# Optimization experiments

Hardware: AMD Instinct MI355X
Metric: run time of the kernel (lower is better)

Reference implementation:

```python
import jax, jax.numpy as jnp
import numpy as np

# Static configuration (mirrors init_kwargs)
F_REAL = 64
F_CAT = 32
OUT = 32
HID = [64, 64, 32]
IDX_REAL_MISS = np.arange(16)   # indices into the real-feature subset
IDX_CAT_MISS = np.arange(8)     # indices into the cat-feature subset
N_CAT_MISS = len(IDX_CAT_MISS)
B = 8192


def wn(v, g):
    """PyTorch weight_norm: w = g * v / ||v|| with norm over input dim (last axis).
    v: [F, out, in], g: [F, out] -> w: [F, out, in]"""
    return g[..., None] * v / jnp.linalg.norm(v, axis=-1, keepdims=True)


def setup_inputs() -> dict:
    key = jax.random.key(0)
    ks = jax.random.split(key, 16)
    s = 0.3
    values = jax.random.normal(ks[0], (B, 96), dtype=jnp.float32)
    miss = (jax.random.uniform(ks[1], (B, 96)) < 0.1).astype(jnp.float32)
    tabular = jnp.stack([values, miss], axis=1)  # [B, 2, 96]
    # Per-feature weight-normed MLP params, stacked over F_REAL features.
    inp = {
        "tabular": tabular,
        "v0": jax.random.normal(ks[2], (F_REAL, HID[0], 1)) * s,
        "g0": jnp.ones((F_REAL, HID[0])),
        "b0": jax.random.normal(ks[3], (F_REAL, HID[0])) * 0.01,
        "v1": jax.random.normal(ks[4], (F_REAL, HID[1], HID[0])) * s,
        "g1": jnp.ones((F_REAL, HID[1])),
        "b1": jax.random.normal(ks[5], (F_REAL, HID[1])) * 0.01,
        "v2": jax.random.normal(ks[6], (F_REAL, HID[2], HID[1])) * s,
        "g2": jnp.ones((F_REAL, HID[2])),
        "b2": jax.random.normal(ks[7], (F_REAL, HID[2])) * 0.01,
        "v3": jax.random.normal(ks[8], (F_REAL, OUT, HID[2])) * s,
        "g3": jnp.ones((F_REAL, OUT)),
        "cat_linear": jax.random.normal(ks[9], (F_CAT, OUT)) * s,
        "missing_emb": jax.random.normal(ks[10], (len(IDX_REAL_MISS) + N_CAT_MISS, OUT)) * s,
        "bias": jnp.zeros((1, OUT)),
    }
    return inp


def reference(tabular, v0, g0, b0, v1, g1, b1, v2, g2, b2, v3, g3,
              cat_linear, missing_emb, bias):
    # Eval mode: nn.Dropout / nn.Dropout1d are identity.
    values, is_missing = tabular[:, 0], tabular[:, 1]
    val_real, miss_real = values[:, :F_REAL], is_missing[:, :F_REAL]
    val_cat, miss_cat = values[:, F_REAL:F_REAL + F_CAT], is_missing[:, F_REAL:F_REAL + F_CAT]

    # Batched tiny MLPs over all real features at once.
    w0 = wn(v0, g0)[:, :, 0]                  # [F, H0] (scalar input)
    h = jax.nn.relu(val_real[:, :, None] * w0[None] + b0[None])        # [B,F,H0]
    h = jax.nn.relu(jnp.einsum('bfi,foi->bfo', h, wn(v1, g1)) + b1[None])  # [B,F,H1]
    h = jax.nn.relu(jnp.einsum('bfi,foi->bfo', h, wn(v2, g2)) + b2[None])  # [B,F,H2]
    feat_real = jnp.einsum('bfi,foi->bfo', h, wn(v3, g3))               # [B,F,OUT]

    feat_cat = cat_linear[None] * val_cat[:, :, None]                   # [B,Fc,OUT]

    feat_real = feat_real * (1.0 - miss_real[:, :, None])
    feat_cat = feat_cat * (1.0 - miss_cat[:, :, None])

    # Scatter-fill missing embeddings (add is exact since masked entries are zero)
    feat_real = feat_real.at[:, IDX_REAL_MISS, :].add(
        missing_emb[N_CAT_MISS:][None] * miss_real[:, IDX_REAL_MISS, None])
    feat_cat = feat_cat.at[:, IDX_CAT_MISS, :].add(
        missing_emb[:N_CAT_MISS][None] * miss_cat[:, IDX_CAT_MISS, None])

    features = jnp.concatenate([feat_real, feat_cat], axis=1)           # [B,96,OUT]
    logits = jnp.sum(features, axis=1) + bias                           # [B,OUT]
    return (logits, features)
```

## Files before the change

kernel.cpp:

```cpp
#include <hip/hip_runtime.h>
#include <math.h>

typedef _Float16 f16;
typedef _Float16 f16x8 __attribute__((ext_vector_type(8)));
typedef float f32x4 __attribute__((ext_vector_type(4)));

#define NB 8192
#define LOGN (NB * 32)

#define OFF_B1 16384
#define OFF_B2 540672
#define OFF_B3 802816
#define OFF_PART 933888

__global__ void prep_weights(const float* __restrict__ v0, const float* __restrict__ g0,
                             const float* __restrict__ v1, const float* __restrict__ g1,
                             const float* __restrict__ v2, const float* __restrict__ g2,
                             const float* __restrict__ v3, const float* __restrict__ g3,
                             float* __restrict__ w0, f16* __restrict__ b1f,
                             f16* __restrict__ b2f, f16* __restrict__ b3f) {
    int t = blockIdx.x * blockDim.x + threadIdx.x;
    if (t < 4096) {
        float v = v0[t];
        w0[t] = g0[t] * (v >= 0.f ? 1.f : -1.f);
    } else if (t < 8192) {
        int r = t - 4096;
        int f = r >> 6, n = r & 63;
        const float* vp = v1 + (size_t)r * 64;
        float ss = 0.f;
        #pragma unroll
        for (int i = 0; i < 64; ++i) ss += vp[i] * vp[i];
        float scale = g1[r] * __frsqrt_rn(ss);
        f16* dst = b1f + f * 4096;
        #pragma unroll
        for (int k = 0; k < 64; ++k) {
            int lane = (n & 15) | (((k & 31) >> 3) << 4);
            dst[(k >> 5) * 2048 + (n >> 4) * 512 + lane * 8 + (k & 7)] = (f16)(vp[k] * scale);
        }
    } else if (t < 10240) {
        int r = t - 8192;
        int f = r >> 5, n = r & 31;
        const float* vp = v2 + (size_t)r * 64;
        float ss = 0.f;
        #pragma unroll
        for (int i = 0; i < 64; ++i) ss += vp[i] * vp[i];
        float scale = g2[r] * __frsqrt_rn(ss);
        f16* dst = b2f + f * 2048;
        #pragma unroll
        for (int k = 0; k < 64; ++k) {
            int lane = (n & 15) | (((k & 31) >> 3) << 4);
            dst[(k >> 5) * 1024 + (n >> 4) * 512 + lane * 8 + (k & 7)] = (f16)(vp[k] * scale);
        }
    } else if (t < 12288) {
        int r = t - 10240;
        int f = r >> 5, n = r & 31;
        const float* vp = v3 + (size_t)r * 32;
        float ss = 0.f;
        #pragma unroll
        for (int i = 0; i < 32; ++i) ss += vp[i] * vp[i];
        float scale = g3[r] * __frsqrt_rn(ss);
        f16* dst = b3f + f * 1024;
        #pragma unroll
        for (int k = 0; k < 32; ++k) {
            int lane = (n & 15) | ((k >> 3) << 4);
            dst[(n >> 4) * 512 + lane * 8 + (k & 7)] = (f16)(vp[k] * scale);
        }
    }
}

__global__ __launch_bounds__(256, 2)
void nam_real_mfma(const float* __restrict__ tab, const float* __restrict__ w0,
                   const f16* __restrict__ b1f, const f16* __restrict__ b2f,
                   const f16* __restrict__ b3f,
                   const float* __restrict__ b0, const float* __restrict__ b1,
                   const float* __restrict__ b2, const float* __restrict__ memb,
                   float* __restrict__ feat, float* __restrict__ part) {
    __shared__ char lds[4][8192];
    const int wave = threadIdx.x >> 6, lane = threadIdx.x & 63;
    const int lq = lane >> 4, lr = lane & 15;
    const int rowbase = blockIdx.x * 128 + wave * 32;
    const int f0 = blockIdx.y * 8;
    char* h1b = lds[wave];
    char* h2b = lds[wave] + 4096;

    float lacc[2][2][4];
    #pragma unroll
    for (int mt = 0; mt < 2; ++mt)
        #pragma unroll
        for (int nt = 0; nt < 2; ++nt)
            #pragma unroll
            for (int j = 0; j < 4; ++j) lacc[mt][nt][j] = 0.f;

    #pragma unroll 1
    for (int fi = 0; fi < 8; ++fi) {
        const int f = f0 + fi;

        f16x8 B1[2][4], B2[2][2], B3[2];
        {
            const f16* p1 = b1f + f * 4096 + lane * 8;
            #pragma unroll
            for (int ks = 0; ks < 2; ++ks)
                #pragma unroll
                for (int nt = 0; nt < 4; ++nt)
                    B1[ks][nt] = *(const f16x8*)(p1 + ks * 2048 + nt * 512);
            const f16* p2 = b2f + f * 2048 + lane * 8;
            #pragma unroll
            for (int ks = 0; ks < 2; ++ks)
                #pragma unroll
                for (int nt = 0; nt < 2; ++nt)
                    B2[ks][nt] = *(const f16x8*)(p2 + ks * 1024 + nt * 512);
            const f16* p3 = b3f + f * 1024 + lane * 8;
            #pragma unroll
            for (int nt = 0; nt < 2; ++nt)
                B3[nt] = *(const f16x8*)(p3 + nt * 512);
        }

        float b1v[4], b2v[2];
        #pragma unroll
        for (int nt = 0; nt < 4; ++nt) b1v[nt] = b1[f * 64 + nt * 16 + lr];
        #pragma unroll
        for (int nt = 0; nt < 2; ++nt) b2v[nt] = b2[f * 32 + nt * 16 + lr];
        float vmt[2];
        #pragma unroll
        for (int mt = 0; mt < 2; ++mt)
            vmt[mt] = tab[(size_t)(rowbase + mt * 16 + lr) * 192 + f];
        float ms[2][4];
        #pragma unroll
        for (int mt = 0; mt < 2; ++mt)
            #pragma unroll
            for (int j = 0; j < 4; ++j)
                ms[mt][j] = tab[(size_t)(rowbase + mt * 16 + lq * 4 + j) * 192 + 96 + f];

        f16x8 A0[2][2];
        #pragma unroll
        for (int ks = 0; ks < 2; ++ks) {
            float w0v[8], b0v[8];
            *(float4*)&w0v[0] = *(const float4*)(w0 + f * 64 + ks * 32 + lq * 8);
            *(float4*)&w0v[4] = *(const float4*)(w0 + f * 64 + ks * 32 + lq * 8 + 4);
            *(float4*)&b0v[0] = *(const float4*)(b0 + f * 64 + ks * 32 + lq * 8);
            *(float4*)&b0v[4] = *(const float4*)(b0 + f * 64 + ks * 32 + lq * 8 + 4);
            #pragma unroll
            for (int mt = 0; mt < 2; ++mt)
                #pragma unroll
                for (int i = 0; i < 8; ++i)
                    A0[mt][ks][i] = (f16)fmaxf(fmaf(vmt[mt], w0v[i], b0v[i]), 0.f);
        }

        f32x4 acc1[2][4];
        #pragma unroll
        for (int mt = 0; mt < 2; ++mt)
            #pragma unroll
            for (int nt = 0; nt < 4; ++nt) acc1[mt][nt] = (f32x4){0.f, 0.f, 0.f, 0.f};
        #pragma unroll
        for (int ks = 0; ks < 2; ++ks)
            #pragma unroll
            for (int nt = 0; nt < 4; ++nt)
                #pragma unroll
                for (int mt = 0; mt < 2; ++mt)
                    acc1[mt][nt] = __builtin_amdgcn_mfma_f32_16x16x32_f16(A0[mt][ks], B1[ks][nt], acc1[mt][nt], 0, 0, 0);
        #pragma unroll
        for (int mt = 0; mt < 2; ++mt)
            #pragma unroll
            for (int nt = 0; nt < 4; ++nt) {
                int n = nt * 16 + lr;
                int colb = ((n >> 3) << 4) + ((n & 7) << 1);
                #pragma unroll
                for (int j = 0; j < 4; ++j) {
                    int row = mt * 16 + lq * 4 + j;
                    int byte = ((row << 7) + colb) ^ ((row & 7) << 4);
                    *(f16*)(h1b + byte) = (f16)fmaxf(acc1[mt][nt][j] + b1v[nt], 0.f);
                }
            }

        f16x8 A1[2][2];
        #pragma unroll
        for (int mt = 0; mt < 2; ++mt)
            #pragma unroll
            for (int ks = 0; ks < 2; ++ks) {
                int row = mt * 16 + lr;
                int byte = ((row << 7) + ((ks * 4 + lq) << 4)) ^ ((row & 7) << 4);
                A1[mt][ks] = *(const f16x8*)(h1b + byte);
            }
        f32x4 acc2[2][2];
        #pragma unroll
        for (int mt = 0; mt < 2; ++mt)
            #pragma unroll
            for (int nt = 0; nt < 2; ++nt) acc2[mt][nt] = (f32x4){0.f, 0.f, 0.f, 0.f};
        #pragma unroll
        for (int ks = 0; ks < 2; ++ks)
            #pragma unroll
            for (int nt = 0; nt < 2; ++nt)
                #pragma unroll
                for (int mt = 0; mt < 2; ++mt)
                    acc2[mt][nt] = __builtin_amdgcn_mfma_f32_16x16x32_f16(A1[mt][ks], B2[ks][nt], acc2[mt][nt], 0, 0, 0);
        #pragma unroll
        for (int mt = 0; mt < 2; ++mt)
            #pragma unroll
            for (int nt = 0; nt < 2; ++nt) {
                int n = nt * 16 + lr;
                int colb = ((n >> 3) << 4) + ((n & 7) << 1);
                #pragma unroll
                for (int j = 0; j < 4; ++j) {
                    int row = mt * 16 + lq * 4 + j;
                    int byte = ((row << 7) + colb) ^ ((row & 7) << 4);
                    *(f16*)(h2b + byte) = (f16)fmaxf(acc2[mt][nt][j] + b2v[nt], 0.f);
                }
            }

        f16x8 A2[2];
        #pragma unroll
        for (int mt = 0; mt < 2; ++mt) {
            int row = mt * 16 + lr;
            int byte = ((row << 7) + (lq << 4)) ^ ((row & 7) << 4);
            A2[mt] = *(const f16x8*)(h2b + byte);
        }
        f32x4 acc3[2][2];
        #pragma unroll
        for (int mt = 0; mt < 2; ++mt)
            #pragma unroll
            for (int nt = 0; nt < 2; ++nt) acc3[mt][nt] = (f32x4){0.f, 0.f, 0.f, 0.f};
        #pragma unroll
        for (int nt = 0; nt < 2; ++nt)
            #pragma unroll
            for (int mt = 0; mt < 2; ++mt)
                acc3[mt][nt] = __builtin_amdgcn_mfma_f32_16x16x32_f16(A2[mt], B3[nt], acc3[mt][nt], 0, 0, 0);

        float e[2] = {0.f, 0.f};
        const bool hasemb = (f < 16);
        if (hasemb) {
            #pragma unroll
            for (int nt = 0; nt < 2; ++nt) e[nt] = memb[(8 + f) * 32 + nt * 16 + lr];
        }
        #pragma unroll
        for (int mt = 0; mt < 2; ++mt)
            #pragma unroll
            for (int nt = 0; nt < 2; ++nt) {
                int o = nt * 16 + lr;
                #pragma unroll
                for (int j = 0; j < 4; ++j) {
                    int row = rowbase + mt * 16 + lq * 4 + j;
                    float keep = 1.f - ms[mt][j];
                    float v = acc3[mt][nt][j] * keep;
                    if (hasemb) v = fmaf(e[nt], ms[mt][j], v);
                    feat[(size_t)row * 3072 + f * 32 + o] = v;
                    lacc[mt][nt][j] += v;
                }
            }
    }

    if (part) {
        float* pp = part + (size_t)blockIdx.y * LOGN;
        #pragma unroll
        for (int mt = 0; mt < 2; ++mt)
            #pragma unroll
            for (int nt = 0; nt < 2; ++nt)
                #pragma unroll
                for (int j = 0; j < 4; ++j) {
                    int row = rowbase + mt * 16 + lq * 4 + j;
                    pp[row * 32 + nt * 16 + lr] = lacc[mt][nt][j];
                }
    }
}

__global__ __launch_bounds__(256)
void nam_cat(const float* __restrict__ tab, const float* __restrict__ cat_linear,
             const float* __restrict__ memb, float* __restrict__ feat,
             float* __restrict__ part) {
    int t = blockIdx.x * blockDim.x + threadIdx.x;
    int o = t & 31;
    int b = t >> 5;
    const float* tb = tab + (size_t)b * 192;
    float sum = 0.f;
    #pragma unroll
    for (int fc = 0; fc < 32; ++fc) {
        float val = tb[64 + fc];
        float miss = tb[160 + fc];
        float r = cat_linear[fc * 32 + o] * val * (1.f - miss);
        if (fc < 8) r = fmaf(memb[fc * 32 + o], miss, r);
        feat[(size_t)b * 3072 + (64 + fc) * 32 + o] = r;
        sum += r;
    }
    if (part) part[8 * LOGN + t] = sum;
}

__global__ __launch_bounds__(256)
void nam_reduce(const float* __restrict__ part, const float* __restrict__ bias,
                float* __restrict__ logits) {
    int t = blockIdx.x * blockDim.x + threadIdx.x;
    float s = bias[t & 31];
    #pragma unroll
    for (int g = 0; g < 9; ++g) s += part[g * LOGN + t];
    logits[t] = s;
}

__global__ __launch_bounds__(256)
void nam_logits(const float* __restrict__ feat, const float* __restrict__ bias,
                float* __restrict__ logits) {
    int t = blockIdx.x * blockDim.x + threadIdx.x;
    int o = t & 31;
    int b = t >> 5;
    float s = bias[o];
    const float* fp = feat + (size_t)b * 3072 + o;
    #pragma unroll 8
    for (int f = 0; f < 96; ++f) s += fp[f * 32];
    logits[t] = s;
}

extern "C" void kernel_launch(void* const* d_in, const int* in_sizes, int n_in,
                              void* d_out, int out_size, void* d_ws, size_t ws_size,
                              hipStream_t stream) {
    const float* tab        = (const float*)d_in[0];
    const float* v0         = (const float*)d_in[1];
    const float* g0         = (const float*)d_in[2];
    const float* b0         = (const float*)d_in[3];
    const float* v1         = (const float*)d_in[4];
    const float* g1         = (const float*)d_in[5];
    const float* b1         = (const float*)d_in[6];
    const float* v2         = (const float*)d_in[7];
    const float* g2         = (const float*)d_in[8];
    const float* b2         = (const float*)d_in[9];
    const float* v3         = (const float*)d_in[10];
    const float* g3         = (const float*)d_in[11];
    const float* cat_linear = (const float*)d_in[12];
    const float* memb       = (const float*)d_in[13];
    const float* bias       = (const float*)d_in[14];

    float* out    = (float*)d_out;
    float* logits = out;
    float* feat   = out + LOGN;

    float* w0  = (float*)d_ws;
    f16*   b1f = (f16*)((char*)d_ws + OFF_B1);
    f16*   b2f = (f16*)((char*)d_ws + OFF_B2);
    f16*   b3f = (f16*)((char*)d_ws + OFF_B3);
    float* part = (float*)((char*)d_ws + OFF_PART);
    const bool use_part = ws_size >= (size_t)OFF_PART + 9ull * LOGN * 4ull;
    float* partp = use_part ? part : nullptr;

    prep_weights<<<48, 256, 0, stream>>>(v0, g0, v1, g1, v2, g2, v3, g3, w0, b1f, b2f, b3f);

    dim3 gr(64, 8);
    nam_real_mfma<<<gr, 256, 0, stream>>>(tab, w0, b1f, b2f, b3f, b0, b1, b2, memb, feat, partp);

    nam_cat<<<LOGN / 256, 256, 0, stream>>>(tab, cat_linear, memb, feat, partp);

    if (use_part)
        nam_reduce<<<LOGN / 256, 256, 0, stream>>>(part, bias, logits);
    else
        nam_logits<<<LOGN / 256, 256, 0, stream>>>(feat, bias, logits);
}
```

Baseline: 53.05 us.

## Split weight prep into parallel passes, stage tab in LDS, fuse cat with reduce

Weight prep is split in two. One kernel computes the per-row norm scales with float4 loads. A second kernel runs one thread per fp16 fragment element, replacing the serial per-row scatter writes. The MFMA kernel now stages its block's value and missing columns in shared memory once, instead of issuing strided global loads on every feature iteration. The categorical kernel also folds in the partial-sum reduction and bias, which removes one launch and one write and re-read of a partial buffer. The cost is an extra prep launch and a __syncthreads.

```diff
diff --git a/kernel.cpp b/kernel.cpp
--- a/kernel.cpp
+++ b/kernel.cpp
@@ -8,63 +8,84 @@
 #define NB 8192
 #define LOGN (NB * 32)
 
-#define OFF_B1 16384
-#define OFF_B2 540672
-#define OFF_B3 802816
-#define OFF_PART 933888
-
-__global__ void prep_weights(const float* __restrict__ v0, const float* __restrict__ g0,
-                             const float* __restrict__ v1, const float* __restrict__ g1,
-                             const float* __restrict__ v2, const float* __restrict__ g2,
-                             const float* __restrict__ v3, const float* __restrict__ g3,
-                             float* __restrict__ w0, f16* __restrict__ b1f,
-                             f16* __restrict__ b2f, f16* __restrict__ b3f) {
+#define OFF_W0   0
+#define OFF_SC1  16384
+#define OFF_SC2  32768
+#define OFF_SC3  40960
+#define OFF_B1   49152
+#define OFF_B2   573440
+#define OFF_B3   835584
+#define OFF_PART 966656
+#define WS_NEED  (OFF_PART + 8ull * LOGN * 4ull)
+
+__global__ __launch_bounds__(256)
+void prep_norm(const float* __restrict__ v0, const float* __restrict__ g0,
+               const float* __restrict__ v1, const float* __restrict__ g1,
+               const float* __restrict__ v2, const float* __restrict__ g2,
+               const float* __restrict__ v3, const float* __restrict__ g3,
+               float* __restrict__ ws) {
     int t = blockIdx.x * blockDim.x + threadIdx.x;
     if (t < 4096) {
         float v = v0[t];
-        w0[t] = g0[t] * (v >= 0.f ? 1.f : -1.f);
+        ws[OFF_W0 / 4 + t] = g0[t] * (v >= 0.f ? 1.f : -1.f);
     } else if (t < 8192) {
         int r = t - 4096;
-        int f = r >> 6, n = r & 63;
         const float* vp = v1 + (size_t)r * 64;
         float ss = 0.f;
         #pragma unroll
-        for (int i = 0; i < 64; ++i) ss += vp[i] * vp[i];
-        float scale = g1[r] * __frsqrt_rn(ss);
-        f16* dst = b1f + f * 4096;
-        #pragma unroll
-        for (int k = 0; k < 64; ++k) {
-            int lane = (n & 15) | (((k & 31) >> 3) << 4);
-            dst[(k >> 5) * 2048 + (n >> 4) * 512 + lane * 8 + (k & 7)] = (f16)(vp[k] * scale);
-        }
+        for (int i = 0; i < 16; ++i) {
+            float4 x = *(const float4*)(vp + i * 4);
+            ss += x.x * x.x + x.y * x.y + x.z * x.z + x.w * x.w;
+        }
+        ws[OFF_SC1 / 4 + r] = g1[r] * __frsqrt_rn(ss);
     } else if (t < 10240) {
         int r = t - 8192;
-        int f = r >> 5, n = r & 31;
         const float* vp = v2 + (size_t)r * 64;
         float ss = 0.f;
         #pragma unroll
-        for (int i = 0; i < 64; ++i) ss += vp[i] * vp[i];
-        float scale = g2[r] * __frsqrt_rn(ss);
-        f16* dst = b2f + f * 2048;
-        #pragma unroll
-        for (int k = 0; k < 64; ++k) {
-            int lane = (n & 15) | (((k & 31) >> 3) << 4);
-            dst[(k >> 5) * 1024 + (n >> 4) * 512 + lane * 8 + (k & 7)] = (f16)(vp[k] * scale);
-        }
+        for (int i = 0; i < 16; ++i) {
+            float4 x = *(const float4*)(vp + i * 4);
+            ss += x.x * x.x + x.y * x.y + x.z * x.z + x.w * x.w;
+        }
+        ws[OFF_SC2 / 4 + r] = g2[r] * __frsqrt_rn(ss);
     } else if (t < 12288) {
         int r = t - 10240;
-        int f = r >> 5, n = r & 31;
         const float* vp = v3 + (size_t)r * 32;
         float ss = 0.f;
         #pragma unroll
-        for (int i = 0; i < 32; ++i) ss += vp[i] * vp[i];
-        float scale = g3[r] * __frsqrt_rn(ss);
-        f16* dst = b3f + f * 1024;
-        #pragma unroll
-        for (int k = 0; k < 32; ++k) {
-            int lane = (n & 15) | ((k >> 3) << 4);
-            dst[(n >> 4) * 512 + lane * 8 + (k & 7)] = (f16)(vp[k] * scale);
-        }
+        for (int i = 0; i < 8; ++i) {
+            float4 x = *(const float4*)(vp + i * 4);
+            ss += x.x * x.x + x.y * x.y + x.z * x.z + x.w * x.w;
+        }
+        ws[OFF_SC3 / 4 + r] = g3[r] * __frsqrt_rn(ss);
+    }
+}
+
+__global__ __launch_bounds__(256)
+void prep_frag(const float* __restrict__ v1, const float* __restrict__ v2,
+               const float* __restrict__ v3, const float* __restrict__ ws,
+               f16* __restrict__ b1f, f16* __restrict__ b2f, f16* __restrict__ b3f) {
+    int t = blockIdx.x * blockDim.x + threadIdx.x;
+    if (t < 262144) {
+        int i = t & 7, lane = (t >> 3) & 63, nt = (t >> 9) & 3, ks = (t >> 11) & 1, f = t >> 12;
+        int k = ks * 32 + ((lane >> 4) << 3) + i;
+        int n = nt * 16 + (lane & 15);
+        int r = f * 64 + n;
+        b1f[t] = (f16)(v1[(size_t)r * 64 + k] * ws[OFF_SC1 / 4 + r]);
+    } else if (t < 393216) {
+        int t2 = t - 262144;
+        int i = t2 & 7, lane = (t2 >> 3) & 63, nt = (t2 >> 9) & 1, ks = (t2 >> 10) & 1, f = t2 >> 11;
+        int k = ks * 32 + ((lane >> 4) << 3) + i;
+        int n = nt * 16 + (lane & 15);
+        int r = f * 32 + n;
+        b2f[t2] = (f16)(v2[(size_t)r * 64 + k] * ws[OFF_SC2 / 4 + r]);
+    } else {
+        int t3 = t - 393216;
+        int i = t3 & 7, lane = (t3 >> 3) & 63, nt = (t3 >> 9) & 1, f = t3 >> 10;
+        int k = ((lane >> 4) << 3) + i;
+        int n = nt * 16 + (lane & 15);
+        int r = f * 32 + n;
+        b3f[t3] = (f16)(v3[(size_t)r * 32 + k] * ws[OFF_SC3 / 4 + r]);
     }
 }
 
@@ -76,6 +97,8 @@
                    const float* __restrict__ b2, const float* __restrict__ memb,
                    float* __restrict__ feat, float* __restrict__ part) {
     __shared__ char lds[4][8192];
+    __shared__ float tv[128][8];
+    __shared__ float tm[128][8];
     const int wave = threadIdx.x >> 6, lane = threadIdx.x & 63;
     const int lq = lane >> 4, lr = lane & 15;
     const int rowbase = blockIdx.x * 128 + wave * 32;
@@ -83,6 +106,16 @@
     char* h1b = lds[wave];
     char* h2b = lds[wave] + 4096;
 
+    #pragma unroll
+    for (int it = 0; it < 8; ++it) {
+        int g = it * 256 + threadIdx.x;
+        int row = g >> 4, w = g & 15;
+        int col = (w < 8) ? (f0 + w) : (96 + f0 + (w - 8));
+        float x = tab[(size_t)(blockIdx.x * 128 + row) * 192 + col];
+        if (w < 8) tv[row][w] = x; else tm[row][w - 8] = x;
+    }
+    __syncthreads();
+
     float lacc[2][2][4];
     #pragma unroll
     for (int mt = 0; mt < 2; ++mt)
@@ -123,13 +156,13 @@
         float vmt[2];
         #pragma unroll
         for (int mt = 0; mt < 2; ++mt)
-            vmt[mt] = tab[(size_t)(rowbase + mt * 16 + lr) * 192 + f];
+            vmt[mt] = tv[wave * 32 + mt * 16 + lr][fi];
         float ms[2][4];
         #pragma unroll
         for (int mt = 0; mt < 2; ++mt)
             #pragma unroll
             for (int j = 0; j < 4; ++j)
-                ms[mt][j] = tab[(size_t)(rowbase + mt * 16 + lq * 4 + j) * 192 + 96 + f];
+                ms[mt][j] = tm[wave * 32 + mt * 16 + lq * 4 + j][fi];
 
         f16x8 A0[2][2];
         #pragma unroll
@@ -263,14 +296,19 @@
 }
 
 __global__ __launch_bounds__(256)
-void nam_cat(const float* __restrict__ tab, const float* __restrict__ cat_linear,
-             const float* __restrict__ memb, float* __restrict__ feat,
-             float* __restrict__ part) {
+void nam_cat_reduce(const float* __restrict__ tab, const float* __restrict__ cat_linear,
+                    const float* __restrict__ memb, const float* __restrict__ bias,
+                    const float* __restrict__ part, float* __restrict__ feat,
+                    float* __restrict__ logits) {
     int t = blockIdx.x * blockDim.x + threadIdx.x;
     int o = t & 31;
     int b = t >> 5;
     const float* tb = tab + (size_t)b * 192;
-    float sum = 0.f;
+    float s = bias[o];
+    if (part) {
+        #pragma unroll
+        for (int g = 0; g < 8; ++g) s += part[g * LOGN + t];
+    }
     #pragma unroll
     for (int fc = 0; fc < 32; ++fc) {
         float val = tb[64 + fc];
@@ -278,19 +316,9 @@
         float r = cat_linear[fc * 32 + o] * val * (1.f - miss);
         if (fc < 8) r = fmaf(memb[fc * 32 + o], miss, r);
         feat[(size_t)b * 3072 + (64 + fc) * 32 + o] = r;
-        sum += r;
-    }
-    if (part) part[8 * LOGN + t] = sum;
-}
-
-__global__ __launch_bounds__(256)
-void nam_reduce(const float* __restrict__ part, const float* __restrict__ bias,
-                float* __restrict__ logits) {
-    int t = blockIdx.x * blockDim.x + threadIdx.x;
-    float s = bias[t & 31];
-    #pragma unroll
-    for (int g = 0; g < 9; ++g) s += part[g * LOGN + t];
-    logits[t] = s;
+        s += r;
+    }
+    if (part) logits[t] = s;
 }
 
 __global__ __launch_bounds__(256)
@@ -329,23 +357,23 @@
     float* logits = out;
     float* feat   = out + LOGN;
 
-    float* w0  = (float*)d_ws;
-    f16*   b1f = (f16*)((char*)d_ws + OFF_B1);
-    f16*   b2f = (f16*)((char*)d_ws + OFF_B2);
-    f16*   b3f = (f16*)((char*)d_ws + OFF_B3);
+    float* ws   = (float*)d_ws;
+    float* w0   = (float*)((char*)d_ws + OFF_W0);
+    f16*   b1f  = (f16*)((char*)d_ws + OFF_B1);
+    f16*   b2f  = (f16*)((char*)d_ws + OFF_B2);
+    f16*   b3f  = (f16*)((char*)d_ws + OFF_B3);
     float* part = (float*)((char*)d_ws + OFF_PART);
-    const bool use_part = ws_size >= (size_t)OFF_PART + 9ull * LOGN * 4ull;
+    const bool use_part = ws_size >= WS_NEED;
     float* partp = use_part ? part : nullptr;
 
-    prep_weights<<<48, 256, 0, stream>>>(v0, g0, v1, g1, v2, g2, v3, g3, w0, b1f, b2f, b3f);
+    prep_norm<<<48, 256, 0, stream>>>(v0, g0, v1, g1, v2, g2, v3, g3, ws);
+    prep_frag<<<1792, 256, 0, stream>>>(v1, v2, v3, ws, b1f, b2f, b3f);
 
     dim3 gr(64, 8);
     nam_real_mfma<<<gr, 256, 0, stream>>>(tab, w0, b1f, b2f, b3f, b0, b1, b2, memb, feat, partp);
 
-    nam_cat<<<LOGN / 256, 256, 0, stream>>>(tab, cat_linear, memb, feat, partp);
-
-    if (use_part)
-        nam_reduce<<<LOGN / 256, 256, 0, stream>>>(part, bias, logits);
-    else
+    nam_cat_reduce<<<LOGN / 256, 256, 0, stream>>>(tab, cat_linear, memb, bias, partp, feat, logits);
+
+    if (!use_part)
         nam_logits<<<LOGN / 256, 256, 0, stream>>>(feat, bias, logits);
 }
```

Measured after the change: 48.00 us. -9.5%, faster.
